# Performance work log

Measured on AMD Instinct MI355X. Metric: run time of the kernel, lower is better.

Reference implementation:

```python
import jax, jax.numpy as jnp
import numpy as np
from jax import lax

V, H = 50257, 256
B, S, T = 128, 50, 32
TQ = 32


def position_encoding(emb):
    # emb: (B, S, T, H); l[s, e] = 1 - s/(T-1) - e/(H-1)*(1 - 2*s/(T-1))
    slen, elen = emb.shape[2], emb.shape[3]
    s = jnp.arange(slen, dtype=jnp.float32)[:, None] / (slen - 1)
    e = jnp.arange(elen, dtype=jnp.float32)[None, :] / (elen - 1)
    l = 1.0 - s - e * (1.0 - 2.0 * s)  # (T, H)
    return jnp.sum(emb * l[None, None], axis=2)  # (B, S, H)


def gru_seq(x, Wih, Whh, bih, bhh):
    # x: (B, T, H); torch GRU cell math; returns outputs (B,T,H), last hidden (B,H)
    h0 = jnp.zeros((x.shape[0], Whh.shape[1]), x.dtype)
    def step(h, xt):
        gi = xt @ Wih.T + bih
        gh = h @ Whh.T + bhh
        ir, iz, inn = jnp.split(gi, 3, axis=-1)
        hr, hz, hn = jnp.split(gh, 3, axis=-1)
        r = jax.nn.sigmoid(ir + hr)
        z = jax.nn.sigmoid(iz + hz)
        n = jnp.tanh(inn + r * hn)
        h_new = (1.0 - z) * n + z * h
        return h_new, h_new
    h_last, ys = lax.scan(step, h0, jnp.swapaxes(x, 0, 1))
    return jnp.swapaxes(ys, 0, 1), h_last


def setup_inputs() -> dict:
    key = jax.random.key(0)
    ks = jax.random.split(key, 16)
    def g(k, shape, scale=0.05):
        return (jax.random.normal(k, shape, dtype=jnp.float32) * scale)
    inp = {
        "contexts": jax.random.randint(ks[0], (B, S, T), 0, V, dtype=jnp.int32),
        "questions": jax.random.randint(ks[1], (B, TQ), 0, V, dtype=jnp.int32),
        "emb": jax.random.uniform(ks[2], (V, H), jnp.float32, -1.0, 1.0),
        "Wih_f": g(ks[3], (3 * H, H)), "Whh_f": g(ks[4], (3 * H, H)),
        "bih_f": jnp.zeros((3 * H,), jnp.float32), "bhh_f": jnp.zeros((3 * H,), jnp.float32),
        "Wih_b": g(ks[5], (3 * H, H)), "Whh_b": g(ks[6], (3 * H, H)),
        "bih_b": jnp.zeros((3 * H,), jnp.float32), "bhh_b": jnp.zeros((3 * H,), jnp.float32),
        "Wih_q": g(ks[7], (3 * H, H)), "Whh_q": g(ks[8], (3 * H, H)),
        "bih_q": jnp.zeros((3 * H,), jnp.float32), "bhh_q": jnp.zeros((3 * H,), jnp.float32),
        "Wo": g(ks[9], (V, H)), "bo": jnp.zeros((V,), jnp.float32),
    }
    return inp


def reference(contexts, questions, emb, Wih_f, Whh_f, bih_f, bhh_f,
              Wih_b, Whh_b, bih_b, bhh_b, Wih_q, Whh_q, bih_q, bhh_q, Wo, bo):
    # InputNet: embed -> position encoding -> bidirectional GRU (halves summed)
    ctx = emb[contexts]                      # (B, S, T, H)
    ctx = position_encoding(ctx)             # (B, S, H)  (dropout = eval no-op)
    out_f, _ = gru_seq(ctx, Wih_f, Whh_f, bih_f, bhh_f)
    out_b, _ = gru_seq(ctx[:, ::-1], Wih_b, Whh_b, bih_b, bhh_b)
    facts = out_f + out_b[:, ::-1]           # (B, S, H)
    # QuestionNet: embed -> GRU, take last hidden
    qemb = emb[questions]                    # (B, TQ, H)
    _, q = gru_seq(qemb, Wih_q, Whh_q, bih_q, bhh_q)   # (B, H)
    # AttnNet: dot-product scores + softmax over sentences (vectorized)
    energies = jnp.einsum('bsd,bd->bs', facts, q)
    attn = jax.nn.softmax(energies, axis=-1)           # (B, S)
    # memory read: bmm(attn, facts)
    read = jnp.einsum('bs,bsd->bd', attn, facts)       # (B, H)
    out = jnp.tanh(q * read) @ Wo.T + bo               # (B, V)
    return out
```

## Files before the change

kernel.cpp:

```cpp
#include <hip/hip_runtime.h>

#define V 50257
#define H 256
#define B 128
#define S 50
#define T 32
#define TQ 32

typedef __bf16 bf16x8 __attribute__((ext_vector_type(8)));
typedef float f32x4 __attribute__((ext_vector_type(4)));

__device__ inline unsigned short f2bf(float x) {
  __bf16 b = (__bf16)x;
  return __builtin_bit_cast(unsigned short, b);
}

__device__ inline float sigf(float x) {
  return 1.f / (1.f + __builtin_amdgcn_exp2f(-1.4426950408889634f * x));
}
__device__ inline float tanhfast(float x) {
  return 1.f - 2.f / (__builtin_amdgcn_exp2f(2.8853900817779268f * x) + 1.f);
}

__global__ __launch_bounds__(256) void k_wconv(
    const float* w0, const float* w1, const float* w2,
    const float* w3, const float* w4, const float* w5,
    unsigned short* dst) {
  int mat = blockIdx.x / 192;
  int blk = blockIdx.x % 192;
  const float* src = (mat == 0) ? w0 : (mat == 1) ? w1 : (mat == 2) ? w2
                   : (mat == 3) ? w3 : (mat == 4) ? w4 : w5;
  int off = blk * 1024 + threadIdx.x * 4;
  float4 v = *(const float4*)(src + off);
  unsigned short* d = dst + mat * 196608 + off;
  d[0] = f2bf(v.x); d[1] = f2bf(v.y); d[2] = f2bf(v.z); d[3] = f2bf(v.w);
}

__global__ __launch_bounds__(256) void k_embed(
    const int* __restrict__ ctx_idx, const int* __restrict__ q_idx,
    const float* __restrict__ emb,
    unsigned short* __restrict__ ctx_bf, unsigned short* __restrict__ q_bf) {
  int tid = threadIdx.x;
  int wv = tid >> 6, lane = tid & 63;
  int r = blockIdx.x * 4 + wv;
  if (r < B * S) {
    int myidx = ctx_idx[r * T + (lane & 31)];
    float e0 = (float)(lane * 4) * (1.f / 255.f);
    float4 acc = make_float4(0.f, 0.f, 0.f, 0.f);
    #pragma unroll 4
    for (int t = 0; t < T; ++t) {
      int id = __shfl(myidx, t, 64);
      float4 v = *(const float4*)&emb[(long)id * H + lane * 4];
      float tf = t * (1.f / 31.f);
      float a = 1.f - tf;
      float bb = 2.f * tf - 1.f;
      acc.x += (a + (e0 + 0.f * (1.f / 255.f)) * bb) * v.x;
      acc.y += (a + (e0 + 1.f * (1.f / 255.f)) * bb) * v.y;
      acc.z += (a + (e0 + 2.f * (1.f / 255.f)) * bb) * v.z;
      acc.w += (a + (e0 + 3.f * (1.f / 255.f)) * bb) * v.w;
    }
    ushort4 o;
    o.x = f2bf(acc.x); o.y = f2bf(acc.y); o.z = f2bf(acc.z); o.w = f2bf(acc.w);
    *(ushort4*)&ctx_bf[r * H + lane * 4] = o;
  } else {
    int rq = r - B * S;
    if (rq < B * TQ) {
      float4 v = *(const float4*)&emb[(long)q_idx[rq] * H + lane * 4];
      ushort4 o;
      o.x = f2bf(v.x); o.y = f2bf(v.y); o.z = f2bf(v.z); o.w = f2bf(v.w);
      *(ushort4*)&q_bf[rq * H + lane * 4] = o;
    }
  }
}

__global__ __launch_bounds__(256) void k_gemm(
    const unsigned short* __restrict__ Xb, const unsigned short* __restrict__ Wb,
    const float* __restrict__ bias, float* __restrict__ Out, int seq) {
  const int n0 = blockIdx.x * 64;
  const int m0 = blockIdx.y * 128;
  __shared__ unsigned short lA[128 * 40];
  __shared__ unsigned short lB[64 * 40];
  int tid = threadIdx.x;
  int lane = tid & 63, wv = tid >> 6;
  int lr = lane & 15, lg = lane >> 4;
  f32x4 acc[2][4] = {};
  int sr = tid >> 2, skk = (tid & 3) * 8;
  for (int kt = 0; kt < 8; ++kt) {
    int k0 = kt * 32;
    __syncthreads();
    *(uint4*)&lA[sr * 40 + skk]        = *(const uint4*)&Xb[(m0 + sr) * 256 + k0 + skk];
    *(uint4*)&lA[(sr + 64) * 40 + skk] = *(const uint4*)&Xb[(m0 + sr + 64) * 256 + k0 + skk];
    *(uint4*)&lB[sr * 40 + skk]        = *(const uint4*)&Wb[(n0 + sr) * 256 + k0 + skk];
    __syncthreads();
    bf16x8 av0 = *(const bf16x8*)&lA[(wv * 32 + lr) * 40 + lg * 8];
    bf16x8 av1 = *(const bf16x8*)&lA[(wv * 32 + 16 + lr) * 40 + lg * 8];
    #pragma unroll
    for (int nt = 0; nt < 4; ++nt) {
      bf16x8 bv = *(const bf16x8*)&lB[(nt * 16 + lr) * 40 + lg * 8];
      acc[0][nt] = __builtin_amdgcn_mfma_f32_16x16x32_bf16(av0, bv, acc[0][nt], 0, 0, 0);
      acc[1][nt] = __builtin_amdgcn_mfma_f32_16x16x32_bf16(av1, bv, acc[1][nt], 0, 0, 0);
    }
  }
  #pragma unroll
  for (int nt = 0; nt < 4; ++nt) {
    int col = n0 + nt * 16 + lr;
    float bs = bias[col];
    #pragma unroll
    for (int mt = 0; mt < 2; ++mt) {
      #pragma unroll
      for (int r = 0; r < 4; ++r) {
        int row = m0 + wv * 32 + mt * 16 + lg * 4 + r;
        int bidx = row / seq;
        int ss = row - bidx * seq;
        Out[(long)(ss * B + bidx) * 768 + col] = acc[mt][nt][r] + bs;
      }
    }
  }
}

__global__ __launch_bounds__(512)
__attribute__((amdgpu_waves_per_eu(2, 2)))
void k_rnn(
    const float* __restrict__ Gf, const float* __restrict__ Gb, const float* __restrict__ Gq,
    const unsigned short* __restrict__ WhF, const unsigned short* __restrict__ WhB,
    const unsigned short* __restrict__ WhQ,
    const float* __restrict__ bhF, const float* __restrict__ bhB, const float* __restrict__ bhQ,
    float* __restrict__ outF, float* __restrict__ outB, float* __restrict__ qvec) {
  int blk = blockIdx.x;
  int mode = blk >> 3;
  int rg = blk & 7;
  const float* G = (mode == 0) ? Gf : (mode == 1) ? Gb : Gq;
  const unsigned short* Wh = (mode == 0) ? WhF : (mode == 1) ? WhB : WhQ;
  const float* bh = (mode == 0) ? bhF : (mode == 1) ? bhB : bhQ;
  const int Tn = (mode == 2) ? TQ : S;
  float* ob = (mode == 0) ? outF : outB;

  __shared__ unsigned short hb[2][16 * 264];

  int tid = threadIdx.x;
  int lane = tid & 63, wv = tid >> 6;
  int lr = lane & 15, lg = lane >> 4;

  for (int i = tid; i < 16 * 264; i += 512) { hb[0][i] = 0; hb[1][i] = 0; }

  f32x4 w[48];
  #pragma unroll
  for (int g = 0; g < 3; ++g)
    #pragma unroll
    for (int nt = 0; nt < 2; ++nt) {
      const unsigned short* wp = Wh + (g * 256 + wv * 32 + nt * 16 + lr) * 256 + lg * 8;
      #pragma unroll
      for (int kt = 0; kt < 8; ++kt)
        w[g * 16 + nt * 8 + kt] = *(const f32x4*)(wp + kt * 32);
    }
  #pragma unroll
  for (int i = 0; i < 48; ++i) asm volatile("" : "+v"(w[i]));

  float bhv[3][2];
  #pragma unroll
  for (int g = 0; g < 3; ++g)
    #pragma unroll
    for (int nt = 0; nt < 2; ++nt)
      bhv[g][nt] = bh[g * 256 + wv * 32 + nt * 16 + lr];

  float hcur[2][4] = {};
  int cur = 0;
  __syncthreads();

  for (int t = 0; t < Tn; ++t) {
    int s = (mode == 1) ? (S - 1 - t) : t;
    const float* Gs = G + (long)s * (128 * 768);
    f32x4 acc[6] = {};
    #pragma unroll
    for (int kt = 0; kt < 8; ++kt) {
      bf16x8 a = *(const bf16x8*)&hb[cur][lr * 264 + kt * 32 + lg * 8];
      #pragma unroll
      for (int g = 0; g < 3; ++g) {
        acc[g * 2 + 0] = __builtin_amdgcn_mfma_f32_16x16x32_bf16(
            a, __builtin_bit_cast(bf16x8, w[g * 16 + kt]), acc[g * 2 + 0], 0, 0, 0);
        acc[g * 2 + 1] = __builtin_amdgcn_mfma_f32_16x16x32_bf16(
            a, __builtin_bit_cast(bf16x8, w[g * 16 + 8 + kt]), acc[g * 2 + 1], 0, 0, 0);
      }
    }
    #pragma unroll
    for (int nt = 0; nt < 2; ++nt) {
      int j = wv * 32 + nt * 16 + lr;
      #pragma unroll
      for (int r = 0; r < 4; ++r) {
        int m = lg * 4 + r;
        long grow = (long)(rg * 16 + m) * 768;
        float xr = Gs[grow + j];
        float xz = Gs[grow + 256 + j];
        float xn = Gs[grow + 512 + j];
        float rr = sigf(xr + acc[0 + nt][r] + bhv[0][nt]);
        float zz = sigf(xz + acc[2 + nt][r] + bhv[1][nt]);
        float nn = tanhfast(xn + rr * (acc[4 + nt][r] + bhv[2][nt]));
        hcur[nt][r] = (1.f - zz) * nn + zz * hcur[nt][r];
      }
    }
    #pragma unroll
    for (int nt = 0; nt < 2; ++nt) {
      int j = wv * 32 + nt * 16 + lr;
      #pragma unroll
      for (int r = 0; r < 4; ++r) {
        int m = lg * 4 + r;
        hb[cur ^ 1][m * 264 + j] = f2bf(hcur[nt][r]);
        if (mode != 2)
          ob[(long)(s * B + rg * 16 + m) * H + j] = hcur[nt][r];
      }
    }
    __syncthreads();
    cur ^= 1;
  }

  if (mode == 2) {
    #pragma unroll
    for (int nt = 0; nt < 2; ++nt) {
      int j = wv * 32 + nt * 16 + lr;
      #pragma unroll
      for (int r = 0; r < 4; ++r) {
        int m = lg * 4 + r;
        qvec[(rg * 16 + m) * H + j] = hcur[nt][r];
      }
    }
  }
}

__global__ __launch_bounds__(256) void k_attn(
    const float* __restrict__ outF, const float* __restrict__ outB,
    const float* __restrict__ qvec, unsigned short* __restrict__ tqv) {
  int b = blockIdx.x, tid = threadIdx.x;
  __shared__ float fs[S * H];
  __shared__ float qs[H];
  __shared__ float es[S];
  qs[tid] = qvec[b * H + tid];
  for (int s = 0; s < S; ++s)
    fs[s * H + tid] = outF[(long)(s * B + b) * H + tid] + outB[(long)(s * B + b) * H + tid];
  __syncthreads();
  int lane = tid & 63, wv = tid >> 6;
  for (int s = wv; s < S; s += 4) {
    const float* fr = &fs[s * H];
    float p = 0.f;
    #pragma unroll
    for (int j = 0; j < 4; ++j) p += fr[lane * 4 + j] * qs[lane * 4 + j];
    #pragma unroll
    for (int off = 32; off > 0; off >>= 1) p += __shfl_xor(p, off, 64);
    if (lane == 0) es[s] = p;
  }
  __syncthreads();
  float mx = -1e30f;
  for (int s = 0; s < S; ++s) mx = fmaxf(mx, es[s]);
  float sum = 0.f;
  for (int s = 0; s < S; ++s) sum += expf(es[s] - mx);
  float inv = 1.f / sum;
  float rd = 0.f;
  for (int s = 0; s < S; ++s) rd += expf(es[s] - mx) * inv * fs[s * H + tid];
  tqv[b * H + tid] = f2bf(tanhf(qs[tid] * rd));
}

__global__ __launch_bounds__(256) void k_out(
    const unsigned short* __restrict__ tqv, const float* __restrict__ Wo,
    const float* __restrict__ bo, float* __restrict__ Out) {
  int n0 = blockIdx.x * 64;
  int tid = threadIdx.x, lane = tid & 63, wv = tid >> 6;
  int lr = lane & 15, lg = lane >> 4;
  __shared__ unsigned short lA[B * H];
  #pragma unroll
  for (int i = 0; i < 16; ++i) {
    int c = tid + i * 256;
    int row = c >> 5, kk = (c & 31) * 8;
    int dst = row * 512 + ((kk * 2) ^ ((row & 7) << 4));
    *(uint4*)((char*)lA + dst) = *(const uint4*)&tqv[row * H + kk];
  }
  __syncthreads();
  int vcol = n0 + wv * 16 + lr;
  int vc = (vcol < V) ? vcol : (V - 1);
  f32x4 acc[8] = {};
  for (int kt = 0; kt < 8; ++kt) {
    const float* wp = &Wo[vc * H + kt * 32 + lg * 8];
    float4 w0 = *(const float4*)wp;
    float4 w1 = *(const float4*)(wp + 4);
    bf16x8 bv;
    bv[0] = (__bf16)w0.x; bv[1] = (__bf16)w0.y; bv[2] = (__bf16)w0.z; bv[3] = (__bf16)w0.w;
    bv[4] = (__bf16)w1.x; bv[5] = (__bf16)w1.y; bv[6] = (__bf16)w1.z; bv[7] = (__bf16)w1.w;
    #pragma unroll
    for (int mt = 0; mt < 8; ++mt) {
      int row = mt * 16 + lr;
      int boff = row * 512 + ((kt * 64 + lg * 16) ^ ((row & 7) << 4));
      bf16x8 av = *(const bf16x8*)((const char*)lA + boff);
      acc[mt] = __builtin_amdgcn_mfma_f32_16x16x32_bf16(av, bv, acc[mt], 0, 0, 0);
    }
  }
  if (vcol < V) {
    float bs = bo[vcol];
    #pragma unroll
    for (int mt = 0; mt < 8; ++mt)
      #pragma unroll
      for (int r = 0; r < 4; ++r) {
        int row = mt * 16 + lg * 4 + r;
        Out[row * V + vcol] = acc[mt][r] + bs;
      }
  }
}

extern "C" void kernel_launch(void* const* d_in, const int* in_sizes, int n_in,
                              void* d_out, int out_size, void* d_ws, size_t ws_size,
                              hipStream_t stream) {
  const int* contexts  = (const int*)d_in[0];
  const int* questions = (const int*)d_in[1];
  const float* emb   = (const float*)d_in[2];
  const float* Wih_f = (const float*)d_in[3];
  const float* Whh_f = (const float*)d_in[4];
  const float* bih_f = (const float*)d_in[5];
  const float* bhh_f = (const float*)d_in[6];
  const float* Wih_b = (const float*)d_in[7];
  const float* Whh_b = (const float*)d_in[8];
  const float* bih_b = (const float*)d_in[9];
  const float* bhh_b = (const float*)d_in[10];
  const float* Wih_q = (const float*)d_in[11];
  const float* Whh_q = (const float*)d_in[12];
  const float* bih_q = (const float*)d_in[13];
  const float* bhh_q = (const float*)d_in[14];
  const float* Wo = (const float*)d_in[15];
  const float* bo = (const float*)d_in[16];
  float* out = (float*)d_out;

  char* ws = (char*)d_ws;
  unsigned short* ctx_bf = (unsigned short*)(ws);
  unsigned short* q_bf   = (unsigned short*)(ws + 3276800);
  unsigned short* wbf    = (unsigned short*)(ws + 5373952);
  unsigned short* WihF_b = wbf + 0 * 196608;
  unsigned short* WhhF_b = wbf + 1 * 196608;
  unsigned short* WihB_b = wbf + 2 * 196608;
  unsigned short* WhhB_b = wbf + 3 * 196608;
  unsigned short* WihQ_b = wbf + 4 * 196608;
  unsigned short* WhhQ_b = wbf + 5 * 196608;
  float* Gf   = (float*)(ws + 7733248);
  float* Gb   = (float*)(ws + 27394048);
  float* Gq   = (float*)(ws + 47054848);
  float* outFp = (float*)(ws + 59637760);
  float* outBp = (float*)(ws + 66191360);
  float* qvec = (float*)(ws + 72744960);
  unsigned short* tqv = (unsigned short*)(ws + 72876032);

  k_wconv<<<1152, 256, 0, stream>>>(Wih_f, Whh_f, Wih_b, Whh_b, Wih_q, Whh_q, wbf);
  k_embed<<<(B * S + B * TQ + 3) / 4, 256, 0, stream>>>(contexts, questions, emb, ctx_bf, q_bf);
  k_gemm<<<dim3(12, 50), 256, 0, stream>>>(ctx_bf, WihF_b, bih_f, Gf, S);
  k_gemm<<<dim3(12, 50), 256, 0, stream>>>(ctx_bf, WihB_b, bih_b, Gb, S);
  k_gemm<<<dim3(12, 32), 256, 0, stream>>>(q_bf, WihQ_b, bih_q, Gq, TQ);
  k_rnn<<<24, 512, 0, stream>>>(Gf, Gb, Gq, WhhF_b, WhhB_b, WhhQ_b,
                                bhh_f, bhh_b, bhh_q, outFp, outBp, qvec);
  k_attn<<<B, 256, 0, stream>>>(outFp, outBp, qvec, tqv);
  k_out<<<786, 256, 0, stream>>>(tqv, Wo, bo, out);
}
```

Measured before the change: 426.2 us.

## Fuse forward/backward input GEMMs, fold hidden biases, prefetch gate inputs in RNN

Reorders the converted weights so the forward and backward input projections form one contiguous 1536-row matrix. The two context GEMMs become a single launch that writes an interleaved gate buffer. The r and z hidden biases are folded into the GEMM epilogue, leaving only the n-gate hidden bias inside the recurrent loop. In the RNN kernel the r/z gate inputs are loaded before the MFMA chain to hide global latency, and the register-pinning asm moves inside the loop with an explicit 256-VGPR budget, which risks spills or a different schedule.

```diff
diff --git a/kernel.cpp b/kernel.cpp
--- a/kernel.cpp
+++ b/kernel.cpp
@@ -75,7 +75,9 @@
 
 __global__ __launch_bounds__(256) void k_gemm(
     const unsigned short* __restrict__ Xb, const unsigned short* __restrict__ Wb,
-    const float* __restrict__ bias, float* __restrict__ Out, int seq) {
+    const float* __restrict__ bia, const float* __restrict__ bha,
+    const float* __restrict__ bib, const float* __restrict__ bhb,
+    float* __restrict__ Out, int seq, int nc) {
   const int n0 = blockIdx.x * 64;
   const int m0 = blockIdx.y * 128;
   __shared__ unsigned short lA[128 * 40];
@@ -104,7 +106,10 @@
   #pragma unroll
   for (int nt = 0; nt < 4; ++nt) {
     int col = n0 + nt * 16 + lr;
-    float bs = bias[col];
+    int local = (col < 768) ? col : col - 768;
+    const float* bi = (col < 768) ? bia : bib;
+    const float* bh = (col < 768) ? bha : bhb;
+    float bs = bi[local] + ((local < 512) ? bh[local] : 0.f);
     #pragma unroll
     for (int mt = 0; mt < 2; ++mt) {
       #pragma unroll
@@ -112,26 +117,27 @@
         int row = m0 + wv * 32 + mt * 16 + lg * 4 + r;
         int bidx = row / seq;
         int ss = row - bidx * seq;
-        Out[(long)(ss * B + bidx) * 768 + col] = acc[mt][nt][r] + bs;
+        Out[(long)(ss * B + bidx) * nc + col] = acc[mt][nt][r] + bs;
       }
     }
   }
 }
 
 __global__ __launch_bounds__(512)
-__attribute__((amdgpu_waves_per_eu(2, 2)))
+__attribute__((amdgpu_waves_per_eu(2, 2), amdgpu_num_vgpr(256)))
 void k_rnn(
-    const float* __restrict__ Gf, const float* __restrict__ Gb, const float* __restrict__ Gq,
-    const unsigned short* __restrict__ WhF, const unsigned short* __restrict__ WhB,
-    const unsigned short* __restrict__ WhQ,
+    const float* __restrict__ Gfb, const float* __restrict__ Gq,
+    const unsigned short* __restrict__ wbf,
     const float* __restrict__ bhF, const float* __restrict__ bhB, const float* __restrict__ bhQ,
     float* __restrict__ outF, float* __restrict__ outB, float* __restrict__ qvec) {
   int blk = blockIdx.x;
   int mode = blk >> 3;
   int rg = blk & 7;
-  const float* G = (mode == 0) ? Gf : (mode == 1) ? Gb : Gq;
-  const unsigned short* Wh = (mode == 0) ? WhF : (mode == 1) ? WhB : WhQ;
-  const float* bh = (mode == 0) ? bhF : (mode == 1) ? bhB : bhQ;
+  const float* G = (mode == 2) ? Gq : Gfb;
+  const int gstride = (mode == 2) ? 768 : 1536;
+  const int goff = (mode == 1) ? 768 : 0;
+  const unsigned short* Wh = wbf + (3 + mode) * 196608;
+  const float* bhn_p = ((mode == 0) ? bhF : (mode == 1) ? bhB : bhQ) + 512;
   const int Tn = (mode == 2) ? TQ : S;
   float* ob = (mode == 0) ? outF : outB;
 
@@ -153,23 +159,35 @@
       for (int kt = 0; kt < 8; ++kt)
         w[g * 16 + nt * 8 + kt] = *(const f32x4*)(wp + kt * 32);
     }
+
+  float bhnv[2];
   #pragma unroll
-  for (int i = 0; i < 48; ++i) asm volatile("" : "+v"(w[i]));
-
-  float bhv[3][2];
-  #pragma unroll
-  for (int g = 0; g < 3; ++g)
-    #pragma unroll
-    for (int nt = 0; nt < 2; ++nt)
-      bhv[g][nt] = bh[g * 256 + wv * 32 + nt * 16 + lr];
+  for (int nt = 0; nt < 2; ++nt)
+    bhnv[nt] = bhn_p[wv * 32 + nt * 16 + lr];
 
   float hcur[2][4] = {};
   int cur = 0;
   __syncthreads();
 
   for (int t = 0; t < Tn; ++t) {
+    #pragma unroll
+    for (int i = 0; i < 48; ++i) asm volatile("" : "+v"(w[i]));
+
     int s = (mode == 1) ? (S - 1 - t) : t;
-    const float* Gs = G + (long)s * (128 * 768);
+    const float* Gs = G + (long)s * (B * gstride) + goff;
+
+    float xr[2][4], xz[2][4];
+    #pragma unroll
+    for (int nt = 0; nt < 2; ++nt) {
+      int j = wv * 32 + nt * 16 + lr;
+      #pragma unroll
+      for (int r = 0; r < 4; ++r) {
+        const float* gp = Gs + (long)(rg * 16 + lg * 4 + r) * gstride + j;
+        xr[nt][r] = gp[0];
+        xz[nt][r] = gp[256];
+      }
+    }
+
     f32x4 acc[6] = {};
     #pragma unroll
     for (int kt = 0; kt < 8; ++kt) {
@@ -182,22 +200,28 @@
             a, __builtin_bit_cast(bf16x8, w[g * 16 + 8 + kt]), acc[g * 2 + 1], 0, 0, 0);
       }
     }
+
+    float rr[2][4], zz[2][4];
+    #pragma unroll
+    for (int nt = 0; nt < 2; ++nt)
+      #pragma unroll
+      for (int r = 0; r < 4; ++r) {
+        rr[nt][r] = sigf(xr[nt][r] + acc[0 + nt][r]);
+        zz[nt][r] = sigf(xz[nt][r] + acc[2 + nt][r]);
+      }
+
     #pragma unroll
     for (int nt = 0; nt < 2; ++nt) {
       int j = wv * 32 + nt * 16 + lr;
       #pragma unroll
       for (int r = 0; r < 4; ++r) {
         int m = lg * 4 + r;
-        long grow = (long)(rg * 16 + m) * 768;
-        float xr = Gs[grow + j];
-        float xz = Gs[grow + 256 + j];
-        float xn = Gs[grow + 512 + j];
-        float rr = sigf(xr + acc[0 + nt][r] + bhv[0][nt]);
-        float zz = sigf(xz + acc[2 + nt][r] + bhv[1][nt]);
-        float nn = tanhfast(xn + rr * (acc[4 + nt][r] + bhv[2][nt]));
-        hcur[nt][r] = (1.f - zz) * nn + zz * hcur[nt][r];
-      }
-    }
+        float xn = Gs[(long)(rg * 16 + m) * gstride + 512 + j];
+        float nn = tanhfast(xn + rr[nt][r] * (acc[4 + nt][r] + bhnv[nt]));
+        hcur[nt][r] = (1.f - zz[nt][r]) * nn + zz[nt][r] * hcur[nt][r];
+      }
+    }
+
     #pragma unroll
     for (int nt = 0; nt < 2; ++nt) {
       int j = wv * 32 + nt * 16 + lr;
@@ -329,27 +353,20 @@
   unsigned short* ctx_bf = (unsigned short*)(ws);
   unsigned short* q_bf   = (unsigned short*)(ws + 3276800);
   unsigned short* wbf    = (unsigned short*)(ws + 5373952);
-  unsigned short* WihF_b = wbf + 0 * 196608;
-  unsigned short* WhhF_b = wbf + 1 * 196608;
-  unsigned short* WihB_b = wbf + 2 * 196608;
-  unsigned short* WhhB_b = wbf + 3 * 196608;
-  unsigned short* WihQ_b = wbf + 4 * 196608;
-  unsigned short* WhhQ_b = wbf + 5 * 196608;
-  float* Gf   = (float*)(ws + 7733248);
-  float* Gb   = (float*)(ws + 27394048);
+  float* Gfb  = (float*)(ws + 7733248);
   float* Gq   = (float*)(ws + 47054848);
   float* outFp = (float*)(ws + 59637760);
   float* outBp = (float*)(ws + 66191360);
   float* qvec = (float*)(ws + 72744960);
   unsigned short* tqv = (unsigned short*)(ws + 72876032);
 
-  k_wconv<<<1152, 256, 0, stream>>>(Wih_f, Whh_f, Wih_b, Whh_b, Wih_q, Whh_q, wbf);
+  k_wconv<<<1152, 256, 0, stream>>>(Wih_f, Wih_b, Wih_q, Whh_f, Whh_b, Whh_q, wbf);
   k_embed<<<(B * S + B * TQ + 3) / 4, 256, 0, stream>>>(contexts, questions, emb, ctx_bf, q_bf);
-  k_gemm<<<dim3(12, 50), 256, 0, stream>>>(ctx_bf, WihF_b, bih_f, Gf, S);
-  k_gemm<<<dim3(12, 50), 256, 0, stream>>>(ctx_bf, WihB_b, bih_b, Gb, S);
-  k_gemm<<<dim3(12, 32), 256, 0, stream>>>(q_bf, WihQ_b, bih_q, Gq, TQ);
-  k_rnn<<<24, 512, 0, stream>>>(Gf, Gb, Gq, WhhF_b, WhhB_b, WhhQ_b,
-                                bhh_f, bhh_b, bhh_q, outFp, outBp, qvec);
+  k_gemm<<<dim3(24, 50), 256, 0, stream>>>(ctx_bf, wbf, bih_f, bhh_f, bih_b, bhh_b,
+                                           Gfb, S, 1536);
+  k_gemm<<<dim3(12, 32), 256, 0, stream>>>(q_bf, wbf + 2 * 196608, bih_q, bhh_q, bih_q, bhh_q,
+                                           Gq, TQ, 768);
+  k_rnn<<<24, 512, 0, stream>>>(Gfb, Gq, wbf, bhh_f, bhh_b, bhh_q, outFp, outBp, qvec);
   k_attn<<<B, 256, 0, stream>>>(outFp, outBp, qvec, tqv);
   k_out<<<786, 256, 0, stream>>>(tqv, Wo, bo, out);
 }
```

Result: slower. 486.3 us (+14.1%).
